# Optimization experiments

Measured on AMD Instinct MI355X. Metric: run time of the kernel, lower is better.

## Reference

```python
import jax, jax.numpy as jnp
import numpy as np

LOG2E = 1.4426950408889634  # log2(e), same constant as the Triton kernel
TEMPERATURE = 0.07
BLK = 1024  # row-block size for blockwise (flash-style) sum-exp accumulation


def setup_inputs() -> dict:
    key = jax.random.key(0)
    k1, k2 = jax.random.split(key)
    B, D = 8192, 512
    return {
        "image_features": jax.random.normal(k1, (B, D), dtype=jnp.float32),
        "text_features": jax.random.normal(k2, (B, D), dtype=jnp.float32),
    }


def reference(image_features, text_features):
    inv_temp = LOG2E / TEMPERATURE  # kernel's inv_temperature (base-2 units)
    # normalized_inputs=False -> L2-normalize along dim=1 (F.normalize)
    Xn = image_features / jnp.linalg.norm(image_features, axis=1, keepdims=True)
    Yn = text_features / jnp.linalg.norm(text_features, axis=1, keepdims=True)
    B = Xn.shape[0]

    # Blockwise accumulation of row/col sums of exp2(S*inv_temp - inv_temp),
    # never materializing the full BxB similarity matrix (mirrors clip_sum_exp_kernel).
    def step(col_sum, x_blk):
        # x_blk: [BLK, D]; E: [BLK, B]
        E = jnp.exp2(x_blk @ Yn.T * inv_temp - inv_temp)
        return col_sum + E.sum(axis=0), E.sum(axis=1)

    col_sum, row_blocks = jax.lax.scan(
        step, jnp.zeros(B, dtype=jnp.float32), Xn.reshape(B // BLK, BLK, -1)
    )
    row_sum = row_blocks.reshape(B)

    # Diagonal (positive-pair) logits, in base-2 units exactly as the source:
    # Sv = <x_i, y_i> * inv_temp - inv_temp
    Sv = jnp.sum(Xn * Yn, axis=-1) * inv_temp - inv_temp
    # Faithful to source: logits = log(exp(Sv)/row_sum) + log(exp(Sv)/col_sum)
    # (note: source uses natural exp on base-2-scaled Sv; log(exp(Sv)/s) == Sv - log(s))
    logits = (Sv - jnp.log(row_sum)) + (Sv - jnp.log(col_sum))
    loss = -jnp.mean(logits) / 2.0
    return loss
```

## Files before the change

kernel.cpp:

```cpp
#include <hip/hip_runtime.h>

#define NB 8192
#define DD 512
#define INV_T 20.609929155556618f

typedef short bf16x8 __attribute__((ext_vector_type(8)));
typedef float f32x4  __attribute__((ext_vector_type(4)));

__device__ static inline unsigned short f2bf(float f) {
  unsigned int u = __float_as_uint(f);
  u += 0x7fff + ((u >> 16) & 1);
  return (unsigned short)(u >> 16);
}

__device__ static inline void async16(void* lds, const void* g) {
  __builtin_amdgcn_global_load_lds(
      (const __attribute__((address_space(1))) unsigned int*)g,
      (__attribute__((address_space(3))) unsigned int*)lds, 16, 0, 0);
}

__global__ __launch_bounds__(256) void norm_kernel(
    const float* __restrict__ X, const float* __restrict__ Y,
    unsigned short* __restrict__ Xnb, unsigned short* __restrict__ Ynb,
    float* __restrict__ Sv) {
  const int wv   = threadIdx.x >> 6;
  const int lane = threadIdx.x & 63;
  const int row  = blockIdx.x * 4 + wv;
  const float4* x4 = (const float4*)(X + (size_t)row * DD);
  const float4* y4 = (const float4*)(Y + (size_t)row * DD);
  float4 xa = x4[lane * 2], xb = x4[lane * 2 + 1];
  float4 ya = y4[lane * 2], yb = y4[lane * 2 + 1];
  float xs[8] = {xa.x, xa.y, xa.z, xa.w, xb.x, xb.y, xb.z, xb.w};
  float ys[8] = {ya.x, ya.y, ya.z, ya.w, yb.x, yb.y, yb.z, yb.w};
  float ssx = 0.f, ssy = 0.f, sxy = 0.f;
#pragma unroll
  for (int k = 0; k < 8; ++k) {
    ssx += xs[k] * xs[k];
    ssy += ys[k] * ys[k];
    sxy += xs[k] * ys[k];
  }
#pragma unroll
  for (int m = 1; m < 64; m <<= 1) {
    ssx += __shfl_xor(ssx, m);
    ssy += __shfl_xor(ssy, m);
    sxy += __shfl_xor(sxy, m);
  }
  const float rnx = 1.0f / sqrtf(ssx);
  const float rny = 1.0f / sqrtf(ssy);
  unsigned short ox[8], oy[8];
#pragma unroll
  for (int k = 0; k < 8; ++k) {
    ox[k] = f2bf(xs[k] * rnx);
    oy[k] = f2bf(ys[k] * rny);
  }
  *(uint4*)(Xnb + (size_t)row * DD + lane * 8) = *(const uint4*)ox;
  *(uint4*)(Ynb + (size_t)row * DD + lane * 8) = *(const uint4*)oy;
  if (lane == 0) Sv[row] = sxy * rnx * rny * INV_T - INV_T;
}

__global__ __launch_bounds__(256) void gemm_kernel(
    const unsigned short* __restrict__ Xnb, const unsigned short* __restrict__ Ynb,
    float* __restrict__ rowp, float* __restrict__ colp) {
  __shared__ __align__(16) char sAB[16384];
  __shared__ float rowpart[2][128];
  __shared__ float colpart[2][128];

  const int t    = threadIdx.x;
  const int wv   = t >> 6;
  const int lane = t & 63;
  const int l16  = lane & 15;
  const int lg   = lane >> 4;
  const int wr   = wv >> 1, wc = wv & 1;
  const int br   = blockIdx.y, bc = blockIdx.x;
  const size_t rowA0 = (size_t)br * 128;
  const size_t rowB0 = (size_t)bc * 128;

  f32x4 acc[4][4] = {};

  for (int kt = 0; kt < 16; ++kt) {
    const int kb = kt * 32;
#pragma unroll
    for (int it = 0; it < 2; ++it) {
      const int obase = it * 4096 + wv * 1024;
      const int o = obase + lane * 16;
      const int r  = o >> 6;
      const int cb = o & 63;
      async16(sAB + obase,        (const char*)(Xnb + (rowA0 + r) * DD + kb) + cb);
      async16(sAB + 8192 + obase, (const char*)(Ynb + (rowB0 + r) * DD + kb) + cb);
    }
    __syncthreads();
    bf16x8 af[4], bfv[4];
#pragma unroll
    for (int i = 0; i < 4; ++i) {
      af[i]  = *(const bf16x8*)(sAB + (wr * 64 + i * 16 + l16) * 64 + lg * 16);
      bfv[i] = *(const bf16x8*)(sAB + 8192 + (wc * 64 + i * 16 + l16) * 64 + lg * 16);
    }
#pragma unroll
    for (int i = 0; i < 4; ++i)
#pragma unroll
      for (int j = 0; j < 4; ++j)
        acc[i][j] = __builtin_amdgcn_mfma_f32_16x16x32_bf16(af[i], bfv[j],
                                                            acc[i][j], 0, 0, 0);
    __syncthreads();
  }

  float colacc[4] = {0.f, 0.f, 0.f, 0.f};
#pragma unroll
  for (int i = 0; i < 4; ++i) {
    float rowacc[4] = {0.f, 0.f, 0.f, 0.f};
#pragma unroll
    for (int j = 0; j < 4; ++j)
#pragma unroll
      for (int r = 0; r < 4; ++r) {
        const float e = exp2f(fmaf(acc[i][j][r], INV_T, -INV_T));
        rowacc[r] += e;
        colacc[j] += e;
      }
#pragma unroll
    for (int r = 0; r < 4; ++r) {
      float v = rowacc[r];
      v += __shfl_xor(v, 1); v += __shfl_xor(v, 2);
      v += __shfl_xor(v, 4); v += __shfl_xor(v, 8);
      if (l16 == 0) rowpart[wc][wr * 64 + i * 16 + lg * 4 + r] = v;
    }
  }
#pragma unroll
  for (int j = 0; j < 4; ++j) {
    float v = colacc[j];
    v += __shfl_xor(v, 16); v += __shfl_xor(v, 32);
    if (lg == 0) colpart[wr][wc * 64 + j * 16 + l16] = v;
  }
  __syncthreads();
  if (t < 128) {
    rowp[(size_t)bc * NB + rowA0 + t] = rowpart[0][t] + rowpart[1][t];
  } else {
    const int c = t - 128;
    colp[(size_t)br * NB + rowB0 + c] = colpart[0][c] + colpart[1][c];
  }
}

__global__ __launch_bounds__(256) void loss_kernel(
    const float* __restrict__ rowp, const float* __restrict__ colp,
    const float* __restrict__ Sv, float* __restrict__ out) {
  __shared__ float wsum[4];
  const int i = blockIdx.x * 256 + threadIdx.x;
  float rs = 0.f, cs = 0.f;
  for (int b = 0; b < 64; ++b) {
    rs += rowp[(size_t)b * NB + i];
    cs += colp[(size_t)b * NB + i];
  }
  float v = 2.f * Sv[i] - logf(rs) - logf(cs);
#pragma unroll
  for (int m = 1; m < 64; m <<= 1) v += __shfl_xor(v, m);
  if ((threadIdx.x & 63) == 0) wsum[threadIdx.x >> 6] = v;
  __syncthreads();
  if (threadIdx.x == 0) {
    const float s = wsum[0] + wsum[1] + wsum[2] + wsum[3];
    atomicAdd(out, s * (-1.0f / (2.0f * NB)));
  }
}

extern "C" void kernel_launch(void* const* d_in, const int* in_sizes, int n_in,
                              void* d_out, int out_size, void* d_ws, size_t ws_size,
                              hipStream_t stream) {
  const float* X = (const float*)d_in[0];
  const float* Y = (const float*)d_in[1];
  char* ws = (char*)d_ws;
  unsigned short* Xnb = (unsigned short*)(ws);
  unsigned short* Ynb = (unsigned short*)(ws + 8388608);
  float* Sv   = (float*)(ws + 16777216);
  float* rowp = (float*)(ws + 16777216 + 32768);
  float* colp = (float*)(ws + 16777216 + 32768 + 2097152);
  float* out  = (float*)d_out;

  hipMemsetAsync(d_out, 0, sizeof(float), stream);
  norm_kernel<<<NB / 4, 256, 0, stream>>>(X, Y, Xnb, Ynb, Sv);
  gemm_kernel<<<dim3(64, 64), 256, 0, stream>>>(Xnb, Ynb, rowp, colp);
  loss_kernel<<<32, 256, 0, stream>>>(rowp, colp, Sv, out);
}
```

Before: 182.7 us.

## Enlarge GEMM tile to 256x256 with double-buffered swizzled LDS pipeline

```diff
diff --git a/kernel.cpp b/kernel.cpp
--- a/kernel.cpp
+++ b/kernel.cpp
@@ -13,7 +13,7 @@
   return (unsigned short)(u >> 16);
 }
 
-__device__ static inline void async16(void* lds, const void* g) {
+__device__ static inline void async16(const void* lds, const void* g) {
   __builtin_amdgcn_global_load_lds(
       (const __attribute__((address_space(1))) unsigned int*)g,
       (__attribute__((address_space(3))) unsigned int*)lds, 16, 0, 0);
@@ -58,84 +58,138 @@
   if (lane == 0) Sv[row] = sxy * rnx * rny * INV_T - INV_T;
 }
 
-__global__ __launch_bounds__(256) void gemm_kernel(
+
+#define STAGE_HALF(SRC, ROW0, LBASE, T) do {                                   \
+  _Pragma("unroll") for (int s_ = 0; s_ < 2; ++s_) {                           \
+    const int Pl_ = s_ * 8192 + tid * 16;                                      \
+    const int L_  = Pl_ ^ (((Pl_ >> 7) & 7) << 4);                             \
+    async16(sT + (LBASE) + s_ * 8192 + wv * 1024,                              \
+            (const char*)(SRC) + (size_t)((ROW0) + (L_ >> 7)) * 1024           \
+              + (T) * 128 + (L_ & 127));                                       \
+  } } while (0)
+
+#define STAGE_A(B_, T_) do {                                                   \
+    STAGE_HALF(Xnb, br * 256,       (B_),         (T_));                       \
+    STAGE_HALF(Xnb, br * 256 + 128, (B_) + 16384, (T_)); } while (0)
+#define STAGE_B(B_, T_) do {                                                   \
+    STAGE_HALF(Ynb, bc * 256,       (B_) + 32768, (T_));                       \
+    STAGE_HALF(Ynb, bc * 256 + 128, (B_) + 49152, (T_)); } while (0)
+
+#define READ_A(B_, MH) do {                                                    \
+  _Pragma("unroll") for (int ks_ = 0; ks_ < 2; ++ks_)                          \
+  _Pragma("unroll") for (int i_ = 0; i_ < 4; ++i_)                             \
+    af[MH][ks_][i_] = *(const bf16x8*)(sT +                                    \
+      (((B_) + aoffL + (MH) * 8192 + i_ * 2048 + ks_ * 64) ^ aswz));           \
+  } while (0)
+
+#define READ_B(B_, J0) do {                                                    \
+  _Pragma("unroll") for (int ks_ = 0; ks_ < 2; ++ks_)                          \
+  _Pragma("unroll") for (int j_ = 0; j_ < 2; ++j_)                             \
+    bfr[ks_][(J0) + j_] = *(const bf16x8*)(sT +                                \
+      (((B_) + boffL + ((J0) + j_) * 2048 + ks_ * 64) ^ aswz));                \
+  } while (0)
+
+#define QUAD(MH, NH) do {                                                      \
+  __builtin_amdgcn_s_setprio(1);                                               \
+  _Pragma("unroll") for (int ks_ = 0; ks_ < 2; ++ks_)                          \
+  _Pragma("unroll") for (int i_ = 0; i_ < 4; ++i_)                             \
+  _Pragma("unroll") for (int j_ = 0; j_ < 2; ++j_)                             \
+    acc[(MH) * 4 + i_][(NH) * 2 + j_] =                                        \
+      __builtin_amdgcn_mfma_f32_16x16x32_bf16(                                 \
+        af[MH][ks_][i_], bfr[ks_][(NH) * 2 + j_],                              \
+        acc[(MH) * 4 + i_][(NH) * 2 + j_], 0, 0, 0);                           \
+  __builtin_amdgcn_s_setprio(0);                                               \
+  } while (0)
+
+__global__ __launch_bounds__(512, 1) void gemm_kernel(
     const unsigned short* __restrict__ Xnb, const unsigned short* __restrict__ Ynb,
     float* __restrict__ rowp, float* __restrict__ colp) {
-  __shared__ __align__(16) char sAB[16384];
-  __shared__ float rowpart[2][128];
-  __shared__ float colpart[2][128];
-
-  const int t    = threadIdx.x;
-  const int wv   = t >> 6;
-  const int lane = t & 63;
+  extern __shared__ __align__(16) char sT[];
+  float* rp = (float*)(sT + 131072);
+  float* cp = (float*)(sT + 131072 + 4096);
+
+  const int tid  = threadIdx.x;
+  const int wv   = tid >> 6;
+  const int lane = tid & 63;
   const int l16  = lane & 15;
   const int lg   = lane >> 4;
-  const int wr   = wv >> 1, wc = wv & 1;
+  const int wr   = wv >> 2, wc = wv & 3;
   const int br   = blockIdx.y, bc = blockIdx.x;
-  const size_t rowA0 = (size_t)br * 128;
-  const size_t rowB0 = (size_t)bc * 128;
-
-  f32x4 acc[4][4] = {};
-
-  for (int kt = 0; kt < 16; ++kt) {
-    const int kb = kt * 32;
-#pragma unroll
-    for (int it = 0; it < 2; ++it) {
-      const int obase = it * 4096 + wv * 1024;
-      const int o = obase + lane * 16;
-      const int r  = o >> 6;
-      const int cb = o & 63;
-      async16(sAB + obase,        (const char*)(Xnb + (rowA0 + r) * DD + kb) + cb);
-      async16(sAB + 8192 + obase, (const char*)(Ynb + (rowB0 + r) * DD + kb) + cb);
+
+  const int aswz  = (l16 & 7) << 4;
+  const int aoffL = (wr * 128 + l16) * 128 + lg * 16;
+  const int boffL = 32768 + (wc * 64 + l16) * 128 + lg * 16;
+
+  f32x4  acc[8][4] = {};
+  bf16x8 af[2][2][4];
+  bf16x8 bfr[2][4];
+
+  STAGE_A(0, 0);
+  STAGE_B(0, 0);
+  asm volatile("s_waitcnt vmcnt(0)" ::: "memory");
+  __builtin_amdgcn_s_barrier();
+  asm volatile("" ::: "memory");
+  READ_A(0, 0);
+  READ_B(0, 0);
+
+  for (int t = 0; t < 8; ++t) {
+    const int base  = (t & 1) << 16;
+    const int other = base ^ (1 << 16);
+    const bool pf   = (t < 7);
+    READ_B(base, 2);
+    if (pf) STAGE_A(other, t + 1);
+    __builtin_amdgcn_s_barrier();
+    QUAD(0, 0);
+    __builtin_amdgcn_s_barrier();
+    READ_A(base, 1);
+    if (pf) STAGE_B(other, t + 1);
+    __builtin_amdgcn_s_barrier();
+    QUAD(0, 1);
+    __builtin_amdgcn_s_barrier();
+    QUAD(1, 0);
+    if (pf) asm volatile("s_waitcnt vmcnt(0)" ::: "memory");
+    asm volatile("s_barrier" ::: "memory");
+    if (pf) {
+      READ_A(other, 0);
+      READ_B(other, 0);
     }
-    __syncthreads();
-    bf16x8 af[4], bfv[4];
-#pragma unroll
-    for (int i = 0; i < 4; ++i) {
-      af[i]  = *(const bf16x8*)(sAB + (wr * 64 + i * 16 + l16) * 64 + lg * 16);
-      bfv[i] = *(const bf16x8*)(sAB + 8192 + (wc * 64 + i * 16 + l16) * 64 + lg * 16);
-    }
-#pragma unroll
-    for (int i = 0; i < 4; ++i)
-#pragma unroll
-      for (int j = 0; j < 4; ++j)
-        acc[i][j] = __builtin_amdgcn_mfma_f32_16x16x32_bf16(af[i], bfv[j],
-                                                            acc[i][j], 0, 0, 0);
-    __syncthreads();
-  }
-
-  float colacc[4] = {0.f, 0.f, 0.f, 0.f};
-#pragma unroll
-  for (int i = 0; i < 4; ++i) {
-    float rowacc[4] = {0.f, 0.f, 0.f, 0.f};
-#pragma unroll
-    for (int j = 0; j < 4; ++j)
+    QUAD(1, 1);
+    __builtin_amdgcn_s_barrier();
+  }
+
+  float cacc[4] = {0.f, 0.f, 0.f, 0.f};
+#pragma unroll
+  for (int I = 0; I < 8; ++I) {
+    float racc[4] = {0.f, 0.f, 0.f, 0.f};
+#pragma unroll
+    for (int J = 0; J < 4; ++J)
 #pragma unroll
       for (int r = 0; r < 4; ++r) {
-        const float e = exp2f(fmaf(acc[i][j][r], INV_T, -INV_T));
-        rowacc[r] += e;
-        colacc[j] += e;
+        const float e = exp2f(fmaf(acc[I][J][r], INV_T, -INV_T));
+        racc[r] += e;
+        cacc[J] += e;
       }
 #pragma unroll
     for (int r = 0; r < 4; ++r) {
-      float v = rowacc[r];
+      float v = racc[r];
       v += __shfl_xor(v, 1); v += __shfl_xor(v, 2);
       v += __shfl_xor(v, 4); v += __shfl_xor(v, 8);
-      if (l16 == 0) rowpart[wc][wr * 64 + i * 16 + lg * 4 + r] = v;
+      if (l16 == 0) rp[wc * 256 + wr * 128 + I * 16 + lg * 4 + r] = v;
     }
   }
 #pragma unroll
-  for (int j = 0; j < 4; ++j) {
-    float v = colacc[j];
+  for (int J = 0; J < 4; ++J) {
+    float v = cacc[J];
     v += __shfl_xor(v, 16); v += __shfl_xor(v, 32);
-    if (lg == 0) colpart[wr][wc * 64 + j * 16 + l16] = v;
+    if (lg == 0) cp[wr * 256 + wc * 64 + J * 16 + l16] = v;
   }
   __syncthreads();
-  if (t < 128) {
-    rowp[(size_t)bc * NB + rowA0 + t] = rowpart[0][t] + rowpart[1][t];
+  if (tid < 256) {
+    rowp[(size_t)bc * NB + br * 256 + tid] =
+        rp[tid] + rp[256 + tid] + rp[512 + tid] + rp[768 + tid];
   } else {
-    const int c = t - 128;
-    colp[(size_t)br * NB + rowB0 + c] = colpart[0][c] + colpart[1][c];
+    const int c = tid - 256;
+    colp[(size_t)br * NB + bc * 256 + c] = cp[c] + cp[256 + c];
   }
 }
 
@@ -145,7 +199,7 @@
   __shared__ float wsum[4];
   const int i = blockIdx.x * 256 + threadIdx.x;
   float rs = 0.f, cs = 0.f;
-  for (int b = 0; b < 64; ++b) {
+  for (int b = 0; b < 32; ++b) {
     rs += rowp[(size_t)b * NB + i];
     cs += colp[(size_t)b * NB + i];
   }
@@ -170,11 +224,15 @@
   unsigned short* Ynb = (unsigned short*)(ws + 8388608);
   float* Sv   = (float*)(ws + 16777216);
   float* rowp = (float*)(ws + 16777216 + 32768);
-  float* colp = (float*)(ws + 16777216 + 32768 + 2097152);
+  float* colp = (float*)(ws + 16777216 + 32768 + 1048576);
   float* out  = (float*)d_out;
+
+  (void)hipFuncSetAttribute((const void*)gemm_kernel,
+                            hipFuncAttributeMaxDynamicSharedMemorySize,
+                            131072 + 6144);
 
   hipMemsetAsync(d_out, 0, sizeof(float), stream);
   norm_kernel<<<NB / 4, 256, 0, stream>>>(X, Y, Xnb, Ynb, Sv);
-  gemm_kernel<<<dim3(64, 64), 256, 0, stream>>>(Xnb, Ynb, rowp, colp);
+  gemm_kernel<<<dim3(32, 32), 512, 131072 + 6144, stream>>>(Xnb, Ynb, rowp, colp);
   loss_kernel<<<32, 256, 0, stream>>>(rowp, colp, Sv, out);
 }
```

New measurement: 182.1 us. Within noise of the previous version (-0.4%).
